# Kernel optimization log

Measured on AMD Instinct MI355X. Metric: run time of the kernel, lower is better.

## Reference

```python
import jax, jax.numpy as jnp
import numpy as np

WIN = 11      # window_size
SIGMA = 1.5
CH = 1        # channel
LEVELS = 5
C1 = 0.01 ** 2
C2 = 0.03 ** 2
MS_WEIGHTS = np.array([0.0448, 0.2856, 0.3001, 0.2363, 0.1333], dtype=np.float32)


def _gaussian_window(dtype):
    x = jnp.arange(WIN, dtype=jnp.float32) - WIN // 2
    g = jnp.exp(-(x ** 2) / (2.0 * SIGMA ** 2))
    g = g / g.sum()
    w2 = jnp.outer(g, g)  # [K, K]
    # depthwise kernel [C, 1, K, K]
    return jnp.broadcast_to(w2[None, None], (CH, 1, WIN, WIN)).astype(dtype)


def _blur(x, w):
    # depthwise 11x11 Gaussian blur, SAME padding (= pad window_size//2)
    return jax.lax.conv_general_dilated(
        x, w, window_strides=(1, 1), padding='SAME',
        dimension_numbers=('NCHW', 'OIHW', 'NCHW'),
        feature_group_count=CH)


def _ssim_level(img1, img2, w):
    mu1 = _blur(img1, w)
    mu2 = _blur(img2, w)
    mu1_sq = mu1 * mu1
    mu2_sq = mu2 * mu2
    mu1_mu2 = mu1 * mu2
    sigma1_sq = _blur(img1 * img1, w) - mu1_sq
    sigma2_sq = _blur(img2 * img2, w) - mu2_sq
    sigma12 = _blur(img1 * img2, w) - mu1_mu2
    denom_c = sigma1_sq + sigma2_sq + C2
    mcs_map = (2.0 * sigma12 + C2) / denom_c
    ssim_map = ((2.0 * mu1_mu2 + C1) / (mu1_sq + mu2_sq + C1)) * mcs_map
    return ssim_map.mean(), mcs_map.mean()


def _avg_pool2(x):
    B, C, H, W = x.shape
    return x.reshape(B, C, H // 2, 2, W // 2, 2).mean(axis=(3, 5))


def reference(img1, img2):
    w = _gaussian_window(img1.dtype)
    weights = jnp.asarray(MS_WEIGHTS, dtype=img1.dtype)
    mssim, mcs = [], []
    for _ in range(LEVELS):  # small fixed loop over pyramid levels
        s, m = _ssim_level(img1, img2, w)
        mssim.append(s)
        mcs.append(m)
        img1 = _avg_pool2(img1)
        img2 = _avg_pool2(img2)
    mssim = jnp.stack(mssim)
    mcs = jnp.stack(mcs)
    return jnp.prod(mcs[:LEVELS - 1] ** weights[:LEVELS - 1]) * mssim[LEVELS - 1] ** weights[LEVELS - 1]


def setup_inputs() -> dict:
    key = jax.random.key(0)
    k1, k2 = jax.random.split(key)
    img1 = jax.random.uniform(k1, (32, 1, 512, 512), dtype=jnp.float32)
    # correlated second image so ssim/mcs means stay positive (fractional powers)
    img2 = jnp.clip(img1 + 0.1 * jax.random.normal(k2, img1.shape, dtype=jnp.float32), 0.0, 1.0)
    return {"img1": img1, "img2": img2}
```

## Files before the change

### kernel.cpp

```cpp
#include <hip/hip_runtime.h>
#include <math.h>


#define TILE 32
#define HALO 5
#define SROWS 42
#define NSLOT 64

struct GaussW { float w[11]; };

#define C1_ (0.01f * 0.01f)
#define C2_ (0.03f * 0.03f)

__global__ __launch_bounds__(256) void pyramid_kernel(
        const float* __restrict__ in1, const float* __restrict__ in2,
        float* __restrict__ l1a, float* __restrict__ l1b,
        float* __restrict__ l2a, float* __restrict__ l2b,
        float* __restrict__ l3a, float* __restrict__ l3b,
        float* __restrict__ l4a, float* __restrict__ l4b) {
    __shared__ float b1[64 * 64], b2[64 * 64];
    __shared__ float c1[32 * 32], c2[32 * 32];
    __shared__ float d1[16 * 16], d2[16 * 16];
    const int tid = threadIdx.x;
    const int n = blockIdx.y;
    const int rx = blockIdx.x & 3, ry = blockIdx.x >> 2;
    const float* p1 = in1 + (size_t)n * 512 * 512;
    const float* p2 = in2 + (size_t)n * 512 * 512;

    for (int i = tid; i < 64 * 32; i += 256) {
        int oy = i >> 5, oxp = i & 31;
        int gy = ry * 128 + 2 * oy, gx = rx * 128 + 4 * oxp;
        float4 r10 = *(const float4*)(p1 + (size_t)gy * 512 + gx);
        float4 r11 = *(const float4*)(p1 + (size_t)(gy + 1) * 512 + gx);
        float4 r20 = *(const float4*)(p2 + (size_t)gy * 512 + gx);
        float4 r21 = *(const float4*)(p2 + (size_t)(gy + 1) * 512 + gx);
        float2 o1 = make_float2(0.25f * (r10.x + r10.y + r11.x + r11.y),
                                0.25f * (r10.z + r10.w + r11.z + r11.w));
        float2 o2 = make_float2(0.25f * (r20.x + r20.y + r21.x + r21.y),
                                0.25f * (r20.z + r20.w + r21.z + r21.w));
        *(float2*)&b1[oy * 64 + 2 * oxp] = o1;
        *(float2*)&b2[oy * 64 + 2 * oxp] = o2;
        size_t o = (size_t)n * 256 * 256 + (size_t)(ry * 64 + oy) * 256 + rx * 64 + 2 * oxp;
        *(float2*)&l1a[o] = o1;
        *(float2*)&l1b[o] = o2;
    }
    __syncthreads();

    for (int i = tid; i < 32 * 16; i += 256) {
        int oy = i >> 4, oxp = i & 15;
        float4 r10 = *(const float4*)&b1[(2 * oy) * 64 + 4 * oxp];
        float4 r11 = *(const float4*)&b1[(2 * oy + 1) * 64 + 4 * oxp];
        float4 r20 = *(const float4*)&b2[(2 * oy) * 64 + 4 * oxp];
        float4 r21 = *(const float4*)&b2[(2 * oy + 1) * 64 + 4 * oxp];
        float2 o1 = make_float2(0.25f * (r10.x + r10.y + r11.x + r11.y),
                                0.25f * (r10.z + r10.w + r11.z + r11.w));
        float2 o2 = make_float2(0.25f * (r20.x + r20.y + r21.x + r21.y),
                                0.25f * (r20.z + r20.w + r21.z + r21.w));
        *(float2*)&c1[oy * 32 + 2 * oxp] = o1;
        *(float2*)&c2[oy * 32 + 2 * oxp] = o2;
        size_t o = (size_t)n * 128 * 128 + (size_t)(ry * 32 + oy) * 128 + rx * 32 + 2 * oxp;
        *(float2*)&l2a[o] = o1;
        *(float2*)&l2b[o] = o2;
    }
    __syncthreads();

    for (int i = tid; i < 16 * 8; i += 256) {
        int oy = i >> 3, oxp = i & 7;
        float4 r10 = *(const float4*)&c1[(2 * oy) * 32 + 4 * oxp];
        float4 r11 = *(const float4*)&c1[(2 * oy + 1) * 32 + 4 * oxp];
        float4 r20 = *(const float4*)&c2[(2 * oy) * 32 + 4 * oxp];
        float4 r21 = *(const float4*)&c2[(2 * oy + 1) * 32 + 4 * oxp];
        float2 o1 = make_float2(0.25f * (r10.x + r10.y + r11.x + r11.y),
                                0.25f * (r10.z + r10.w + r11.z + r11.w));
        float2 o2 = make_float2(0.25f * (r20.x + r20.y + r21.x + r21.y),
                                0.25f * (r20.z + r20.w + r21.z + r21.w));
        *(float2*)&d1[oy * 16 + 2 * oxp] = o1;
        *(float2*)&d2[oy * 16 + 2 * oxp] = o2;
        size_t o = (size_t)n * 64 * 64 + (size_t)(ry * 16 + oy) * 64 + rx * 16 + 2 * oxp;
        *(float2*)&l3a[o] = o1;
        *(float2*)&l3b[o] = o2;
    }
    __syncthreads();

    for (int i = tid; i < 8 * 4; i += 256) {
        int oy = i >> 2, oxp = i & 3;
        float4 r10 = *(const float4*)&d1[(2 * oy) * 16 + 4 * oxp];
        float4 r11 = *(const float4*)&d1[(2 * oy + 1) * 16 + 4 * oxp];
        float4 r20 = *(const float4*)&d2[(2 * oy) * 16 + 4 * oxp];
        float4 r21 = *(const float4*)&d2[(2 * oy + 1) * 16 + 4 * oxp];
        float2 o1 = make_float2(0.25f * (r10.x + r10.y + r11.x + r11.y),
                                0.25f * (r10.z + r10.w + r11.z + r11.w));
        float2 o2 = make_float2(0.25f * (r20.x + r20.y + r21.x + r21.y),
                                0.25f * (r20.z + r20.w + r21.z + r21.w));
        size_t o = (size_t)n * 32 * 32 + (size_t)(ry * 8 + oy) * 32 + rx * 8 + 2 * oxp;
        *(float2*)&l4a[o] = o1;
        *(float2*)&l4b[o] = o2;
    }
}

__global__ __launch_bounds__(256, 4) void ssim_all_kernel(
        const float* __restrict__ i0a, const float* __restrict__ i0b,
        const float* __restrict__ l1a, const float* __restrict__ l1b,
        const float* __restrict__ l2a, const float* __restrict__ l2b,
        const float* __restrict__ l3a, const float* __restrict__ l3b,
        const float* __restrict__ l4a, const float* __restrict__ l4b,
        float* __restrict__ acc,
        GaussW gw) {
    __shared__ float hbuf[5][SROWS * TILE];
    __shared__ float red_s[4], red_m[4];

    const int tid = threadIdx.x;
    const int t = blockIdx.x;
    const int n = blockIdx.y;
    int level, idx, W;
    const float* base1;
    const float* base2;
    if (t < 256)      { level = 0; idx = t;       W = 512; base1 = i0a; base2 = i0b; }
    else if (t < 320) { level = 1; idx = t - 256; W = 256; base1 = l1a; base2 = l1b; }
    else if (t < 336) { level = 2; idx = t - 320; W = 128; base1 = l2a; base2 = l2b; }
    else if (t < 340) { level = 3; idx = t - 336; W = 64;  base1 = l3a; base2 = l3b; }
    else              { level = 4; idx = 0;       W = 32;  base1 = l4a; base2 = l4b; }
    const int tpr = W >> 5;
    const int sh = 31 - __clz(tpr);
    const int tile_x = (idx & (tpr - 1)) << 5;
    const int tile_y = (idx >> sh) << 5;
    const float* p1 = base1 + (size_t)n * W * W;
    const float* p2 = base2 + (size_t)n * W * W;

    for (int it = tid; it < SROWS * 8; it += 256) {
        int r = it >> 3, c4 = it & 7;
        int gy = tile_y + r - HALO;
        int gx0 = tile_x + (c4 << 2) - 8;
        bool rowok = (gy >= 0) && (gy < W);
        const float* row1 = p1 + (size_t)gy * W;
        const float* row2 = p2 + (size_t)gy * W;
        float a1[20], a2[20];
#pragma unroll
        for (int q = 0; q < 5; q++) {
            int g = gx0 + q * 4;
            bool ok = rowok && (g >= 0) && (g + 4 <= W);
            float4 v1 = ok ? *(const float4*)(row1 + g) : make_float4(0.f, 0.f, 0.f, 0.f);
            float4 v2 = ok ? *(const float4*)(row2 + g) : make_float4(0.f, 0.f, 0.f, 0.f);
            a1[q * 4 + 0] = v1.x; a1[q * 4 + 1] = v1.y; a1[q * 4 + 2] = v1.z; a1[q * 4 + 3] = v1.w;
            a2[q * 4 + 0] = v2.x; a2[q * 4 + 1] = v2.y; a2[q * 4 + 2] = v2.z; a2[q * 4 + 3] = v2.w;
        }
        float p11[14], p22[14], p12[14];
#pragma unroll
        for (int i = 0; i < 14; i++) {
            float u = a1[i + 3], v = a2[i + 3];
            p11[i] = u * u;
            p22[i] = v * v;
            p12[i] = u * v;
        }
        float h0[4] = {0, 0, 0, 0}, h1[4] = {0, 0, 0, 0}, h2[4] = {0, 0, 0, 0};
        float h3[4] = {0, 0, 0, 0}, h4[4] = {0, 0, 0, 0};
#pragma unroll
        for (int k = 0; k < 11; k++) {
            float wk = gw.w[k];
#pragma unroll
            for (int j = 0; j < 4; j++) {
                h0[j] += wk * a1[3 + j + k];
                h1[j] += wk * a2[3 + j + k];
                h2[j] += wk * p11[j + k];
                h3[j] += wk * p22[j + k];
                h4[j] += wk * p12[j + k];
            }
        }
        int ob = r * TILE + (c4 << 2);
        *(float4*)&hbuf[0][ob] = make_float4(h0[0], h0[1], h0[2], h0[3]);
        *(float4*)&hbuf[1][ob] = make_float4(h1[0], h1[1], h1[2], h1[3]);
        *(float4*)&hbuf[2][ob] = make_float4(h2[0], h2[1], h2[2], h2[3]);
        *(float4*)&hbuf[3][ob] = make_float4(h3[0], h3[1], h3[2], h3[3]);
        *(float4*)&hbuf[4][ob] = make_float4(h4[0], h4[1], h4[2], h4[3]);
    }
    __syncthreads();

    float ssim_v = 0.f, mcs_v = 0.f;
    {
        int tx = tid & 31, ty4 = tid >> 5;
        int y0 = ty4 * 4;
        float m[5][4];
#pragma unroll
        for (int ch = 0; ch < 5; ch++) {
            float v[14];
#pragma unroll
            for (int r = 0; r < 14; r++) v[r] = hbuf[ch][(y0 + r) * TILE + tx];
#pragma unroll
            for (int j = 0; j < 4; j++) {
                float s = 0.f;
#pragma unroll
                for (int k = 0; k < 11; k++) s += gw.w[k] * v[j + k];
                m[ch][j] = s;
            }
        }
#pragma unroll
        for (int j = 0; j < 4; j++) {
            float mu1 = m[0][j], mu2 = m[1][j];
            float mu1sq = mu1 * mu1, mu2sq = mu2 * mu2, mu12 = mu1 * mu2;
            float sg11 = m[2][j] - mu1sq;
            float sg22 = m[3][j] - mu2sq;
            float sg12 = m[4][j] - mu12;
            float mcs  = (2.f * sg12 + C2_) / (sg11 + sg22 + C2_);
            float ssim = ((2.f * mu12 + C1_) / (mu1sq + mu2sq + C1_)) * mcs;
            ssim_v += ssim;
            mcs_v  += mcs;
        }
    }

#pragma unroll
    for (int off = 32; off > 0; off >>= 1) {
        ssim_v += __shfl_down(ssim_v, off);
        mcs_v  += __shfl_down(mcs_v, off);
    }
    int wave = tid >> 6, lane = tid & 63;
    if (lane == 0) { red_s[wave] = ssim_v; red_m[wave] = mcs_v; }
    __syncthreads();
    if (tid == 0) {
        float S = red_s[0] + red_s[1] + red_s[2] + red_s[3];
        float M = red_m[0] + red_m[1] + red_m[2] + red_m[3];
        unsigned slot = ((unsigned)(t << 5) + (unsigned)n) & (NSLOT - 1);
        float* a = acc + level * 2 * NSLOT;
        atomicAdd(&a[slot], S);
        atomicAdd(&a[NSLOT + slot], M);
    }
}

__global__ void finalize_kernel(const float* __restrict__ acc,
                                float* __restrict__ out, int N) {
    int lane = threadIdx.x & 63;
    float sums[10];
#pragma unroll
    for (int q = 0; q < 10; q++) {
        float v = acc[q * NSLOT + lane];
#pragma unroll
        for (int off = 32; off > 0; off >>= 1) v += __shfl_down(v, off);
        sums[q] = v;
    }
    if (blockIdx.x == 0 && threadIdx.x == 0) {
        const float wts[5] = {0.0448f, 0.2856f, 0.3001f, 0.2363f, 0.1333f};
        float r = 1.f;
#pragma unroll
        for (int l = 0; l < 5; l++) {
            int Hl = 512 >> l;
            float cnt = (float)N * (float)Hl * (float)Hl;
            float ssim_m = sums[2 * l] / cnt;
            float mcs_m  = sums[2 * l + 1] / cnt;
            if (l < 4) r *= powf(mcs_m, wts[l]);
            else       r *= powf(ssim_m, wts[4]);
        }
        out[0] = r;
    }
}

extern "C" void kernel_launch(void* const* d_in, const int* in_sizes, int n_in,
                              void* d_out, int out_size, void* d_ws, size_t ws_size,
                              hipStream_t stream) {
    const float* img1 = (const float*)d_in[0];
    const float* img2 = (const float*)d_in[1];
    float* out = (float*)d_out;
    const int HW0 = 512 * 512;
    const int N = in_sizes[0] / HW0;

    float* base = (float*)d_ws;
    float* acc = base;
    size_t cur = 10 * NSLOT;
    float* w1[5] = {nullptr};
    float* w2[5] = {nullptr};
    for (int l = 1; l < 5; l++) {
        int Hl = 512 >> l;
        size_t hw = (size_t)Hl * Hl;
        w1[l] = base + cur; cur += (size_t)N * hw;
        w2[l] = base + cur; cur += (size_t)N * hw;
    }

    hipMemsetAsync(acc, 0, 10 * NSLOT * sizeof(float), stream);

    GaussW gw;
    {
        double g[11], sum = 0.0;
        for (int i = 0; i < 11; i++) {
            double x = (double)(i - 5);
            g[i] = exp(-(x * x) / (2.0 * 1.5 * 1.5));
            sum += g[i];
        }
        for (int i = 0; i < 11; i++) gw.w[i] = (float)(g[i] / sum);
    }

    pyramid_kernel<<<dim3(16, N), 256, 0, stream>>>(
        img1, img2, w1[1], w2[1], w1[2], w2[2], w1[3], w2[3], w1[4], w2[4]);

    ssim_all_kernel<<<dim3(341, N), 256, 0, stream>>>(
        img1, img2, w1[1], w2[1], w1[2], w2[2], w1[3], w2[3], w1[4], w2[4],
        acc, gw);

    finalize_kernel<<<1, 64, 0, stream>>>(acc, out, N);
}
```

Measured before the change: 177.7 us.

## Fuse pyramid build with level-0 SSIM and pack channel pairs into float2 vectors

Merges the pyramid downsampling into the same launch as the level-0 SSIM tiles. Pyramid regions shrink to 64x64 and run as extra blocks, so the full-resolution SSIM work no longer waits on a separate pyramid kernel. The coarser levels run in a second, smaller launch. The blur code also packs image pairs and their squares into 2-wide vectors, which may allow packed FMA, and adds an unchecked fast path for interior tiles. The added level-0 blocks reread the full-resolution input, and the split gives an extra launch boundary at the coarse levels.

```diff
diff --git a/kernel.cpp b/kernel.cpp
--- a/kernel.cpp
+++ b/kernel.cpp
@@ -1,6 +1,8 @@
 #include <hip/hip_runtime.h>
 #include <math.h>
 
+
+typedef float v2f __attribute__((ext_vector_type(2)));
 
 #define TILE 32
 #define HALO 5
@@ -12,24 +14,174 @@
 #define C1_ (0.01f * 0.01f)
 #define C2_ (0.03f * 0.03f)
 
-__global__ __launch_bounds__(256) void pyramid_kernel(
+#define SMEM_FLOATS 6728
+
+__device__ __forceinline__ void ssim_tile(
+        const float* __restrict__ p1, const float* __restrict__ p2,
+        int W, int tile_x, int tile_y, const GaussW& gw,
+        float* __restrict__ accL, unsigned slot, float* smem, int tid) {
+    v2f* hb01 = (v2f*)smem;
+    v2f* hb23 = (v2f*)(smem + 2 * SROWS * TILE);
+    float* hb4 = smem + 4 * SROWS * TILE;
+    float* red = smem + 5 * SROWS * TILE;
+
+    const bool xfast = (tile_x >= 8) && (tile_x + TILE + 8 <= W);
+
+    for (int it = tid; it < SROWS * 8; it += 256) {
+        int r = it >> 3, c4 = it & 7;
+        int gy = tile_y + r - HALO;
+        int gx0 = tile_x + (c4 << 2) - 8;
+        bool rowok = (gy >= 0) && (gy < W);
+        const float* row1 = p1 + (size_t)gy * W;
+        const float* row2 = p2 + (size_t)gy * W;
+        float a1[20], a2[20];
+#pragma unroll
+        for (int i = 0; i < 20; i++) { a1[i] = 0.f; a2[i] = 0.f; }
+        if (xfast) {
+            if (rowok) {
+#pragma unroll
+                for (int q = 0; q < 5; q++) {
+                    float4 v1 = *(const float4*)(row1 + gx0 + q * 4);
+                    float4 v2v = *(const float4*)(row2 + gx0 + q * 4);
+                    a1[q*4+0] = v1.x;  a1[q*4+1] = v1.y;  a1[q*4+2] = v1.z;  a1[q*4+3] = v1.w;
+                    a2[q*4+0] = v2v.x; a2[q*4+1] = v2v.y; a2[q*4+2] = v2v.z; a2[q*4+3] = v2v.w;
+                }
+            }
+        } else {
+#pragma unroll
+            for (int q = 0; q < 5; q++) {
+                int g = gx0 + q * 4;
+                if (rowok && g >= 0 && g + 4 <= W) {
+                    float4 v1 = *(const float4*)(row1 + g);
+                    float4 v2v = *(const float4*)(row2 + g);
+                    a1[q*4+0] = v1.x;  a1[q*4+1] = v1.y;  a1[q*4+2] = v1.z;  a1[q*4+3] = v1.w;
+                    a2[q*4+0] = v2v.x; a2[q*4+1] = v2v.y; a2[q*4+2] = v2v.z; a2[q*4+3] = v2v.w;
+                }
+            }
+        }
+        v2f A[20];
+#pragma unroll
+        for (int i = 0; i < 20; i++) A[i] = (v2f){a1[i], a2[i]};
+        v2f P[14];
+        float p12[14];
+#pragma unroll
+        for (int i = 0; i < 14; i++) {
+            v2f u = A[i + 3];
+            P[i] = u * u;
+            p12[i] = u.x * u.y;
+        }
+        v2f h01[4] = {(v2f)(0.f), (v2f)(0.f), (v2f)(0.f), (v2f)(0.f)};
+        v2f h23[4] = {(v2f)(0.f), (v2f)(0.f), (v2f)(0.f), (v2f)(0.f)};
+        float h4[4] = {0.f, 0.f, 0.f, 0.f};
+#pragma unroll
+        for (int k = 0; k < 11; k++) {
+            float wk = gw.w[k];
+#pragma unroll
+            for (int j = 0; j < 4; j++) {
+                h01[j] += wk * A[3 + j + k];
+                h23[j] += wk * P[j + k];
+                h4[j]  += wk * p12[j + k];
+            }
+        }
+        int ob = r * TILE + (c4 << 2);
+#pragma unroll
+        for (int j = 0; j < 4; j++) { hb01[ob + j] = h01[j]; hb23[ob + j] = h23[j]; }
+        *(float4*)&hb4[ob] = make_float4(h4[0], h4[1], h4[2], h4[3]);
+    }
+    __syncthreads();
+
+    float ssim_v = 0.f, mcs_v = 0.f;
+    {
+        int tx = tid & 31, y0 = (tid >> 5) * 4;
+        v2f m01[4], m23[4];
+        float m4[4];
+        {
+            v2f v[14];
+#pragma unroll
+            for (int r = 0; r < 14; r++) v[r] = hb01[(y0 + r) * TILE + tx];
+#pragma unroll
+            for (int j = 0; j < 4; j++) {
+                v2f s = (v2f)(0.f);
+#pragma unroll
+                for (int k = 0; k < 11; k++) s += gw.w[k] * v[j + k];
+                m01[j] = s;
+            }
+        }
+        {
+            v2f v[14];
+#pragma unroll
+            for (int r = 0; r < 14; r++) v[r] = hb23[(y0 + r) * TILE + tx];
+#pragma unroll
+            for (int j = 0; j < 4; j++) {
+                v2f s = (v2f)(0.f);
+#pragma unroll
+                for (int k = 0; k < 11; k++) s += gw.w[k] * v[j + k];
+                m23[j] = s;
+            }
+        }
+        {
+            float v[14];
+#pragma unroll
+            for (int r = 0; r < 14; r++) v[r] = hb4[(y0 + r) * TILE + tx];
+#pragma unroll
+            for (int j = 0; j < 4; j++) {
+                float s = 0.f;
+#pragma unroll
+                for (int k = 0; k < 11; k++) s += gw.w[k] * v[j + k];
+                m4[j] = s;
+            }
+        }
+#pragma unroll
+        for (int j = 0; j < 4; j++) {
+            float mu1 = m01[j].x, mu2 = m01[j].y;
+            float mu1sq = mu1 * mu1, mu2sq = mu2 * mu2, mu12 = mu1 * mu2;
+            float sg11 = m23[j].x - mu1sq;
+            float sg22 = m23[j].y - mu2sq;
+            float sg12 = m4[j] - mu12;
+            float mcs  = (2.f * sg12 + C2_) / (sg11 + sg22 + C2_);
+            float ssim = ((2.f * mu12 + C1_) / (mu1sq + mu2sq + C1_)) * mcs;
+            ssim_v += ssim;
+            mcs_v  += mcs;
+        }
+    }
+
+#pragma unroll
+    for (int off = 32; off > 0; off >>= 1) {
+        ssim_v += __shfl_down(ssim_v, off);
+        mcs_v  += __shfl_down(mcs_v, off);
+    }
+    int wave = tid >> 6, lane = tid & 63;
+    if (lane == 0) { red[wave] = ssim_v; red[4 + wave] = mcs_v; }
+    __syncthreads();
+    if (tid == 0) {
+        float S = red[0] + red[1] + red[2] + red[3];
+        float M = red[4] + red[5] + red[6] + red[7];
+        atomicAdd(&accL[slot], S);
+        atomicAdd(&accL[NSLOT + slot], M);
+    }
+}
+
+__device__ __forceinline__ void pyramid_region(
         const float* __restrict__ in1, const float* __restrict__ in2,
+        int n, int reg,
         float* __restrict__ l1a, float* __restrict__ l1b,
         float* __restrict__ l2a, float* __restrict__ l2b,
         float* __restrict__ l3a, float* __restrict__ l3b,
-        float* __restrict__ l4a, float* __restrict__ l4b) {
-    __shared__ float b1[64 * 64], b2[64 * 64];
-    __shared__ float c1[32 * 32], c2[32 * 32];
-    __shared__ float d1[16 * 16], d2[16 * 16];
-    const int tid = threadIdx.x;
-    const int n = blockIdx.y;
-    const int rx = blockIdx.x & 3, ry = blockIdx.x >> 2;
+        float* __restrict__ l4a, float* __restrict__ l4b,
+        float* smem, int tid) {
+    float* b1 = smem;
+    float* b2 = smem + 1024;
+    float* c1 = smem + 2048;
+    float* c2 = smem + 2304;
+    float* d1 = smem + 2560;
+    float* d2 = smem + 2624;
+    const int rx = reg & 7, ry = reg >> 3;
     const float* p1 = in1 + (size_t)n * 512 * 512;
     const float* p2 = in2 + (size_t)n * 512 * 512;
 
-    for (int i = tid; i < 64 * 32; i += 256) {
-        int oy = i >> 5, oxp = i & 31;
-        int gy = ry * 128 + 2 * oy, gx = rx * 128 + 4 * oxp;
+    for (int i = tid; i < 32 * 16; i += 256) {
+        int oy = i >> 4, oxp = i & 15;
+        int gy = ry * 64 + 2 * oy, gx = rx * 64 + 4 * oxp;
         float4 r10 = *(const float4*)(p1 + (size_t)gy * 512 + gx);
         float4 r11 = *(const float4*)(p1 + (size_t)(gy + 1) * 512 + gx);
         float4 r20 = *(const float4*)(p2 + (size_t)gy * 512 + gx);
@@ -38,191 +190,114 @@
                                 0.25f * (r10.z + r10.w + r11.z + r11.w));
         float2 o2 = make_float2(0.25f * (r20.x + r20.y + r21.x + r21.y),
                                 0.25f * (r20.z + r20.w + r21.z + r21.w));
-        *(float2*)&b1[oy * 64 + 2 * oxp] = o1;
-        *(float2*)&b2[oy * 64 + 2 * oxp] = o2;
-        size_t o = (size_t)n * 256 * 256 + (size_t)(ry * 64 + oy) * 256 + rx * 64 + 2 * oxp;
+        *(float2*)&b1[oy * 32 + 2 * oxp] = o1;
+        *(float2*)&b2[oy * 32 + 2 * oxp] = o2;
+        size_t o = (size_t)n * 256 * 256 + (size_t)(ry * 32 + oy) * 256 + rx * 32 + 2 * oxp;
         *(float2*)&l1a[o] = o1;
         *(float2*)&l1b[o] = o2;
     }
     __syncthreads();
-
-    for (int i = tid; i < 32 * 16; i += 256) {
-        int oy = i >> 4, oxp = i & 15;
-        float4 r10 = *(const float4*)&b1[(2 * oy) * 64 + 4 * oxp];
-        float4 r11 = *(const float4*)&b1[(2 * oy + 1) * 64 + 4 * oxp];
-        float4 r20 = *(const float4*)&b2[(2 * oy) * 64 + 4 * oxp];
-        float4 r21 = *(const float4*)&b2[(2 * oy + 1) * 64 + 4 * oxp];
+    if (tid < 16 * 8) {
+        int oy = tid >> 3, oxp = tid & 7;
+        float4 r10 = *(const float4*)&b1[(2 * oy) * 32 + 4 * oxp];
+        float4 r11 = *(const float4*)&b1[(2 * oy + 1) * 32 + 4 * oxp];
+        float4 r20 = *(const float4*)&b2[(2 * oy) * 32 + 4 * oxp];
+        float4 r21 = *(const float4*)&b2[(2 * oy + 1) * 32 + 4 * oxp];
         float2 o1 = make_float2(0.25f * (r10.x + r10.y + r11.x + r11.y),
                                 0.25f * (r10.z + r10.w + r11.z + r11.w));
         float2 o2 = make_float2(0.25f * (r20.x + r20.y + r21.x + r21.y),
                                 0.25f * (r20.z + r20.w + r21.z + r21.w));
-        *(float2*)&c1[oy * 32 + 2 * oxp] = o1;
-        *(float2*)&c2[oy * 32 + 2 * oxp] = o2;
-        size_t o = (size_t)n * 128 * 128 + (size_t)(ry * 32 + oy) * 128 + rx * 32 + 2 * oxp;
+        *(float2*)&c1[oy * 16 + 2 * oxp] = o1;
+        *(float2*)&c2[oy * 16 + 2 * oxp] = o2;
+        size_t o = (size_t)n * 128 * 128 + (size_t)(ry * 16 + oy) * 128 + rx * 16 + 2 * oxp;
         *(float2*)&l2a[o] = o1;
         *(float2*)&l2b[o] = o2;
     }
     __syncthreads();
-
-    for (int i = tid; i < 16 * 8; i += 256) {
-        int oy = i >> 3, oxp = i & 7;
-        float4 r10 = *(const float4*)&c1[(2 * oy) * 32 + 4 * oxp];
-        float4 r11 = *(const float4*)&c1[(2 * oy + 1) * 32 + 4 * oxp];
-        float4 r20 = *(const float4*)&c2[(2 * oy) * 32 + 4 * oxp];
-        float4 r21 = *(const float4*)&c2[(2 * oy + 1) * 32 + 4 * oxp];
+    if (tid < 8 * 4) {
+        int oy = tid >> 2, oxp = tid & 3;
+        float4 r10 = *(const float4*)&c1[(2 * oy) * 16 + 4 * oxp];
+        float4 r11 = *(const float4*)&c1[(2 * oy + 1) * 16 + 4 * oxp];
+        float4 r20 = *(const float4*)&c2[(2 * oy) * 16 + 4 * oxp];
+        float4 r21 = *(const float4*)&c2[(2 * oy + 1) * 16 + 4 * oxp];
         float2 o1 = make_float2(0.25f * (r10.x + r10.y + r11.x + r11.y),
                                 0.25f * (r10.z + r10.w + r11.z + r11.w));
         float2 o2 = make_float2(0.25f * (r20.x + r20.y + r21.x + r21.y),
                                 0.25f * (r20.z + r20.w + r21.z + r21.w));
-        *(float2*)&d1[oy * 16 + 2 * oxp] = o1;
-        *(float2*)&d2[oy * 16 + 2 * oxp] = o2;
-        size_t o = (size_t)n * 64 * 64 + (size_t)(ry * 16 + oy) * 64 + rx * 16 + 2 * oxp;
+        *(float2*)&d1[oy * 8 + 2 * oxp] = o1;
+        *(float2*)&d2[oy * 8 + 2 * oxp] = o2;
+        size_t o = (size_t)n * 64 * 64 + (size_t)(ry * 8 + oy) * 64 + rx * 8 + 2 * oxp;
         *(float2*)&l3a[o] = o1;
         *(float2*)&l3b[o] = o2;
     }
     __syncthreads();
-
-    for (int i = tid; i < 8 * 4; i += 256) {
-        int oy = i >> 2, oxp = i & 3;
-        float4 r10 = *(const float4*)&d1[(2 * oy) * 16 + 4 * oxp];
-        float4 r11 = *(const float4*)&d1[(2 * oy + 1) * 16 + 4 * oxp];
-        float4 r20 = *(const float4*)&d2[(2 * oy) * 16 + 4 * oxp];
-        float4 r21 = *(const float4*)&d2[(2 * oy + 1) * 16 + 4 * oxp];
+    if (tid < 4 * 2) {
+        int oy = tid >> 1, oxp = tid & 1;
+        float4 r10 = *(const float4*)&d1[(2 * oy) * 8 + 4 * oxp];
+        float4 r11 = *(const float4*)&d1[(2 * oy + 1) * 8 + 4 * oxp];
+        float4 r20 = *(const float4*)&d2[(2 * oy) * 8 + 4 * oxp];
+        float4 r21 = *(const float4*)&d2[(2 * oy + 1) * 8 + 4 * oxp];
         float2 o1 = make_float2(0.25f * (r10.x + r10.y + r11.x + r11.y),
                                 0.25f * (r10.z + r10.w + r11.z + r11.w));
         float2 o2 = make_float2(0.25f * (r20.x + r20.y + r21.x + r21.y),
                                 0.25f * (r20.z + r20.w + r21.z + r21.w));
-        size_t o = (size_t)n * 32 * 32 + (size_t)(ry * 8 + oy) * 32 + rx * 8 + 2 * oxp;
+        size_t o = (size_t)n * 32 * 32 + (size_t)(ry * 4 + oy) * 32 + rx * 4 + 2 * oxp;
         *(float2*)&l4a[o] = o1;
         *(float2*)&l4b[o] = o2;
     }
 }
 
-__global__ __launch_bounds__(256, 4) void ssim_all_kernel(
+__global__ __launch_bounds__(256, 4) void d1_kernel(
         const float* __restrict__ i0a, const float* __restrict__ i0b,
+        float* __restrict__ l1a, float* __restrict__ l1b,
+        float* __restrict__ l2a, float* __restrict__ l2b,
+        float* __restrict__ l3a, float* __restrict__ l3b,
+        float* __restrict__ l4a, float* __restrict__ l4b,
+        float* __restrict__ acc, GaussW gw) {
+    __shared__ float smem[SMEM_FLOATS];
+    const int tid = threadIdx.x;
+    const int t = blockIdx.x;
+    const int n = blockIdx.y;
+    if (t < 64) {
+        pyramid_region(i0a, i0b, n, t, l1a, l1b, l2a, l2b, l3a, l3b, l4a, l4b,
+                       smem, tid);
+    } else {
+        int idx = t - 64;
+        int tile_x = (idx & 15) << 5;
+        int tile_y = (idx >> 4) << 5;
+        const float* p1 = i0a + (size_t)n * 512 * 512;
+        const float* p2 = i0b + (size_t)n * 512 * 512;
+        unsigned slot = ((unsigned)(idx << 5) + (unsigned)n) & (NSLOT - 1);
+        ssim_tile(p1, p2, 512, tile_x, tile_y, gw, acc, slot, smem, tid);
+    }
+}
+
+__global__ __launch_bounds__(256, 4) void d2_kernel(
         const float* __restrict__ l1a, const float* __restrict__ l1b,
         const float* __restrict__ l2a, const float* __restrict__ l2b,
         const float* __restrict__ l3a, const float* __restrict__ l3b,
         const float* __restrict__ l4a, const float* __restrict__ l4b,
-        float* __restrict__ acc,
-        GaussW gw) {
-    __shared__ float hbuf[5][SROWS * TILE];
-    __shared__ float red_s[4], red_m[4];
-
+        float* __restrict__ acc, GaussW gw) {
+    __shared__ float smem[SMEM_FLOATS];
     const int tid = threadIdx.x;
     const int t = blockIdx.x;
     const int n = blockIdx.y;
     int level, idx, W;
     const float* base1;
     const float* base2;
-    if (t < 256)      { level = 0; idx = t;       W = 512; base1 = i0a; base2 = i0b; }
-    else if (t < 320) { level = 1; idx = t - 256; W = 256; base1 = l1a; base2 = l1b; }
-    else if (t < 336) { level = 2; idx = t - 320; W = 128; base1 = l2a; base2 = l2b; }
-    else if (t < 340) { level = 3; idx = t - 336; W = 64;  base1 = l3a; base2 = l3b; }
-    else              { level = 4; idx = 0;       W = 32;  base1 = l4a; base2 = l4b; }
+    if (t < 64)      { level = 1; idx = t;      W = 256; base1 = l1a; base2 = l1b; }
+    else if (t < 80) { level = 2; idx = t - 64; W = 128; base1 = l2a; base2 = l2b; }
+    else if (t < 84) { level = 3; idx = t - 80; W = 64;  base1 = l3a; base2 = l3b; }
+    else             { level = 4; idx = 0;      W = 32;  base1 = l4a; base2 = l4b; }
     const int tpr = W >> 5;
     const int sh = 31 - __clz(tpr);
     const int tile_x = (idx & (tpr - 1)) << 5;
     const int tile_y = (idx >> sh) << 5;
     const float* p1 = base1 + (size_t)n * W * W;
     const float* p2 = base2 + (size_t)n * W * W;
-
-    for (int it = tid; it < SROWS * 8; it += 256) {
-        int r = it >> 3, c4 = it & 7;
-        int gy = tile_y + r - HALO;
-        int gx0 = tile_x + (c4 << 2) - 8;
-        bool rowok = (gy >= 0) && (gy < W);
-        const float* row1 = p1 + (size_t)gy * W;
-        const float* row2 = p2 + (size_t)gy * W;
-        float a1[20], a2[20];
-#pragma unroll
-        for (int q = 0; q < 5; q++) {
-            int g = gx0 + q * 4;
-            bool ok = rowok && (g >= 0) && (g + 4 <= W);
-            float4 v1 = ok ? *(const float4*)(row1 + g) : make_float4(0.f, 0.f, 0.f, 0.f);
-            float4 v2 = ok ? *(const float4*)(row2 + g) : make_float4(0.f, 0.f, 0.f, 0.f);
-            a1[q * 4 + 0] = v1.x; a1[q * 4 + 1] = v1.y; a1[q * 4 + 2] = v1.z; a1[q * 4 + 3] = v1.w;
-            a2[q * 4 + 0] = v2.x; a2[q * 4 + 1] = v2.y; a2[q * 4 + 2] = v2.z; a2[q * 4 + 3] = v2.w;
-        }
-        float p11[14], p22[14], p12[14];
-#pragma unroll
-        for (int i = 0; i < 14; i++) {
-            float u = a1[i + 3], v = a2[i + 3];
-            p11[i] = u * u;
-            p22[i] = v * v;
-            p12[i] = u * v;
-        }
-        float h0[4] = {0, 0, 0, 0}, h1[4] = {0, 0, 0, 0}, h2[4] = {0, 0, 0, 0};
-        float h3[4] = {0, 0, 0, 0}, h4[4] = {0, 0, 0, 0};
-#pragma unroll
-        for (int k = 0; k < 11; k++) {
-            float wk = gw.w[k];
-#pragma unroll
-            for (int j = 0; j < 4; j++) {
-                h0[j] += wk * a1[3 + j + k];
-                h1[j] += wk * a2[3 + j + k];
-                h2[j] += wk * p11[j + k];
-                h3[j] += wk * p22[j + k];
-                h4[j] += wk * p12[j + k];
-            }
-        }
-        int ob = r * TILE + (c4 << 2);
-        *(float4*)&hbuf[0][ob] = make_float4(h0[0], h0[1], h0[2], h0[3]);
-        *(float4*)&hbuf[1][ob] = make_float4(h1[0], h1[1], h1[2], h1[3]);
-        *(float4*)&hbuf[2][ob] = make_float4(h2[0], h2[1], h2[2], h2[3]);
-        *(float4*)&hbuf[3][ob] = make_float4(h3[0], h3[1], h3[2], h3[3]);
-        *(float4*)&hbuf[4][ob] = make_float4(h4[0], h4[1], h4[2], h4[3]);
-    }
-    __syncthreads();
-
-    float ssim_v = 0.f, mcs_v = 0.f;
-    {
-        int tx = tid & 31, ty4 = tid >> 5;
-        int y0 = ty4 * 4;
-        float m[5][4];
-#pragma unroll
-        for (int ch = 0; ch < 5; ch++) {
-            float v[14];
-#pragma unroll
-            for (int r = 0; r < 14; r++) v[r] = hbuf[ch][(y0 + r) * TILE + tx];
-#pragma unroll
-            for (int j = 0; j < 4; j++) {
-                float s = 0.f;
-#pragma unroll
-                for (int k = 0; k < 11; k++) s += gw.w[k] * v[j + k];
-                m[ch][j] = s;
-            }
-        }
-#pragma unroll
-        for (int j = 0; j < 4; j++) {
-            float mu1 = m[0][j], mu2 = m[1][j];
-            float mu1sq = mu1 * mu1, mu2sq = mu2 * mu2, mu12 = mu1 * mu2;
-            float sg11 = m[2][j] - mu1sq;
-            float sg22 = m[3][j] - mu2sq;
-            float sg12 = m[4][j] - mu12;
-            float mcs  = (2.f * sg12 + C2_) / (sg11 + sg22 + C2_);
-            float ssim = ((2.f * mu12 + C1_) / (mu1sq + mu2sq + C1_)) * mcs;
-            ssim_v += ssim;
-            mcs_v  += mcs;
-        }
-    }
-
-#pragma unroll
-    for (int off = 32; off > 0; off >>= 1) {
-        ssim_v += __shfl_down(ssim_v, off);
-        mcs_v  += __shfl_down(mcs_v, off);
-    }
-    int wave = tid >> 6, lane = tid & 63;
-    if (lane == 0) { red_s[wave] = ssim_v; red_m[wave] = mcs_v; }
-    __syncthreads();
-    if (tid == 0) {
-        float S = red_s[0] + red_s[1] + red_s[2] + red_s[3];
-        float M = red_m[0] + red_m[1] + red_m[2] + red_m[3];
-        unsigned slot = ((unsigned)(t << 5) + (unsigned)n) & (NSLOT - 1);
-        float* a = acc + level * 2 * NSLOT;
-        atomicAdd(&a[slot], S);
-        atomicAdd(&a[NSLOT + slot], M);
-    }
+    unsigned slot = ((unsigned)(t << 5) + (unsigned)n) & (NSLOT - 1);
+    ssim_tile(p1, p2, W, tile_x, tile_y, gw, acc + level * 2 * NSLOT, slot,
+              smem, tid);
 }
 
 __global__ void finalize_kernel(const float* __restrict__ acc,
@@ -286,12 +361,10 @@
         for (int i = 0; i < 11; i++) gw.w[i] = (float)(g[i] / sum);
     }
 
-    pyramid_kernel<<<dim3(16, N), 256, 0, stream>>>(
-        img1, img2, w1[1], w2[1], w1[2], w2[2], w1[3], w2[3], w1[4], w2[4]);
-
-    ssim_all_kernel<<<dim3(341, N), 256, 0, stream>>>(
+    d1_kernel<<<dim3(320, N), 256, 0, stream>>>(
         img1, img2, w1[1], w2[1], w1[2], w2[2], w1[3], w2[3], w1[4], w2[4],
         acc, gw);
-
+    d2_kernel<<<dim3(85, N), 256, 0, stream>>>(
+        w1[1], w2[1], w1[2], w2[2], w1[3], w2[3], w1[4], w2[4], acc, gw);
     finalize_kernel<<<1, 64, 0, stream>>>(acc, out, N);
 }
```

Result: faster. 173.1 us (-2.6%).
